# Optimization experiments

Hardware: AMD Instinct MI355X
Metric: run time of the kernel (lower is better)

The kernel has to match this reference:

```python
import jax, jax.numpy as jnp
import numpy as np

DIM = 1024
NQ = 16
NKV = 4
HD = DIM // NQ  # 64
HID = 2048
E = 8
B, S = 1, 1024
EPS = 1e-6


def rmsnorm(x, w):
    ms = jnp.mean(x * x, axis=-1, keepdims=True)
    return w * (x * jax.lax.rsqrt(ms + EPS))


def rope_tables(seq_len, head_dim):
    inv_freq = 1.0 / (10000.0 ** (jnp.arange(0, head_dim, 2, dtype=jnp.float32) / head_dim))
    t = jnp.arange(seq_len, dtype=jnp.float32)
    freqs = jnp.einsum('i,j->ij', t, inv_freq)  # [S, HD/2]
    return jnp.cos(freqs), jnp.sin(freqs)


def apply_rope(x, cos, sin):
    # x: [B, S, H, HD]; cos/sin: [S, HD/2]
    c = cos[None, :, None, :]
    s = sin[None, :, None, :]
    half = x.shape[-1] // 2
    x1, x2 = x[..., :half], x[..., half:]
    return jnp.concatenate([x1 * c - x2 * s, x1 * s + x2 * c], axis=-1)


def setup_inputs() -> dict:
    key = jax.random.key(0)
    ks = jax.random.split(key, 20)
    sc = lambda fan_in: 1.0 / np.sqrt(fan_in)
    d = {}
    d['x'] = jax.random.normal(ks[0], (B, S, DIM), dtype=jnp.float32)
    d['ln1_w'] = jnp.ones((DIM,), jnp.float32)
    d['ln2_w'] = jnp.ones((DIM,), jnp.float32)
    d['Wq'] = jax.random.normal(ks[1], (DIM, DIM), jnp.float32) * sc(DIM)
    d['bq'] = jnp.zeros((DIM,), jnp.float32)
    d['Wk'] = jax.random.normal(ks[2], (DIM, HD * NKV), jnp.float32) * sc(DIM)
    d['bk'] = jnp.zeros((HD * NKV,), jnp.float32)
    d['Wv'] = jax.random.normal(ks[3], (DIM, HD * NKV), jnp.float32) * sc(DIM)
    d['bv'] = jnp.zeros((HD * NKV,), jnp.float32)
    d['qn_w'] = jnp.ones((HD,), jnp.float32)
    d['kn_w'] = jnp.ones((HD,), jnp.float32)
    d['Wg'] = jax.random.normal(ks[4], (HD, HD), jnp.float32) * sc(HD)
    d['bg'] = jnp.zeros((HD,), jnp.float32)
    d['Wo'] = jax.random.normal(ks[5], (DIM, DIM), jnp.float32) * sc(DIM)
    d['bo'] = jnp.zeros((DIM,), jnp.float32)
    d['Wr'] = jax.random.normal(ks[6], (DIM, E), jnp.float32) * sc(DIM)
    d['br'] = jnp.zeros((E,), jnp.float32)
    d['W1'] = jax.random.normal(ks[7], (E, DIM, 2 * HID), jnp.float32) * sc(DIM)
    d['b1'] = jnp.zeros((E, 2 * HID), jnp.float32)
    d['W2'] = jax.random.normal(ks[8], (E, HID, DIM), jnp.float32) * sc(HID)
    d['b2'] = jnp.zeros((E, DIM), jnp.float32)
    return d


def _forward(x, ln1_w, ln2_w, Wq, bq, Wk, bk, Wv, bv, qn_w, kn_w, Wg, bg, Wo, bo,
             Wr, br, W1, b1, W2, b2):
    batch, seq, _ = x.shape
    cos, sin = rope_tables(seq, HD)

    # --- attention ---
    h = rmsnorm(x, ln1_w)
    q = (h @ Wq + bq).reshape(batch, seq, NQ, HD)
    k = (h @ Wk + bk).reshape(batch, seq, NKV, HD)
    v = (h @ Wv + bv).reshape(batch, seq, NKV, HD)
    q = rmsnorm(apply_rope(q, cos, sin), qn_w)
    k = rmsnorm(apply_rope(k, cos, sin), kn_w)
    rep = NQ // NKV
    k = jnp.repeat(k, rep, axis=2)  # [B,S,NQ,HD]
    v = jnp.repeat(v, rep, axis=2)
    scores = jnp.einsum('bthd,bshd->bhts', q, k) / np.sqrt(HD)
    causal = jnp.tril(jnp.ones((seq, seq), dtype=bool))
    scores = jnp.where(causal[None, None], scores, -jnp.inf)
    attn = jax.nn.softmax(scores, axis=-1)
    out = jnp.einsum('bhts,bshd->bthd', attn, v)
    gate = jax.nn.sigmoid(out @ Wg + bg)
    out = (out * gate).reshape(batch, seq, DIM)
    x = x + out @ Wo + bo

    # --- top-1 MoE (note: output is NOT scaled by router probs) ---
    h2 = rmsnorm(x, ln2_w)
    logits = h2 @ Wr + br  # [B,S,E]
    top1 = jnp.argmax(logits, axis=-1).reshape(-1)  # [T]
    xt = h2.reshape(-1, DIM)  # [T,DIM]
    # dense dispatch: run all experts, gather the chosen one
    u = jnp.einsum('td,edf->tef', xt, W1) + b1  # [T,E,2H]
    u1, u2 = u[..., :HID], u[..., HID:]
    act = u1 * jax.nn.sigmoid(u2)  # SwiGLU
    y_all = jnp.einsum('teh,ehd->ted', act, W2) + b2  # [T,E,DIM]
    y = jnp.take_along_axis(y_all, top1[:, None, None], axis=1)[:, 0, :]
    return x + y.reshape(batch, seq, DIM)


def reference(x, ln1_w, ln2_w, Wq, bq, Wk, bk, Wv, bv, qn_w, kn_w, Wg, bg, Wo, bo,
              Wr, br, W1, b1, W2, b2):
    return _forward(x, ln1_w, ln2_w, Wq, bq, Wk, bk, Wv, bv, qn_w, kn_w,
                    Wg, bg, Wo, bo, Wr, br, W1, b1, W2, b2)
```

## Files before the change

### kernel.cpp

```cpp
#include <hip/hip_runtime.h>
#include <hip/hip_bf16.h>
#include <cstddef>

#define DIM 1024
#define NQ 16
#define NKV 4
#define HD 64
#define HID 2048
#define NE 8
#define SEQ 1024
#define EPSF 1e-6f
#define MAX_TILES 24
#define GST 72

typedef __hip_bfloat16 bf16;
typedef __attribute__((ext_vector_type(8))) short short8;
typedef __attribute__((ext_vector_type(4))) float floatx4;

typedef union { short8 s; unsigned int u[4]; } s8u;

__device__ __forceinline__ unsigned int f2b(float f) {
    union { bf16 b; unsigned short s; } u;
    u.b = __float2bfloat16(f);
    return (unsigned int)u.s;
}
__device__ __forceinline__ unsigned int pk2(float a, float b) {
    return f2b(a) | (f2b(b) << 16);
}

__global__ __launch_bounds__(256) void rmsnorm_kernel(const float* __restrict__ src,
                                                      const float* __restrict__ w,
                                                      float* __restrict__ dst)
{
    int row = blockIdx.x, tid = threadIdx.x;
    __shared__ float red[256];
    float vals[4];
    float sq = 0.f;
    size_t base = (size_t)row * DIM;
    #pragma unroll
    for (int i = 0; i < 4; i++) {
        int idx = tid + i * 256;
        float v = src[base + idx];
        vals[i] = v; sq += v * v;
    }
    red[tid] = sq; __syncthreads();
    for (int s = 128; s > 0; s >>= 1) {
        if (tid < s) red[tid] += red[tid + s];
        __syncthreads();
    }
    float rs = 1.0f / sqrtf(red[0] * (1.0f / DIM) + EPSF);
    #pragma unroll
    for (int i = 0; i < 4; i++) {
        int idx = tid + i * 256;
        dst[base + idx] = w[idx] * vals[i] * rs;
    }
}

__global__ __launch_bounds__(256) void gemm_kernel(
    const float* __restrict__ A, const float* __restrict__ B, const float* __restrict__ bias,
    float* __restrict__ C, const float* __restrict__ resf,
    const int* __restrict__ perm, const int* __restrict__ tile_expert,
    int N, int K, int mode)
{
    __shared__ short As[64 * GST];
    __shared__ short Bs[64 * GST];
    int tid = threadIdx.x;
    int mbase = blockIdx.y * 64, nbase = blockIdx.x * 64;

    size_t Beoff = 0, biasoff = 0;
    if (tile_expert) {
        int e = tile_expert[blockIdx.y];
        if (e < 0) return;
        Beoff = (size_t)e * K * N;
        biasoff = (size_t)e * N;
    }

    int ar = tid >> 4, ak = (tid & 15) << 2;
    int bn = tid & 63, bkk = (tid >> 6) << 4;
    const float* BpBase = B + Beoff + (size_t)bkk * N + nbase + bn;

    int wv = tid >> 6, ln = tid & 63;
    int fm = (wv << 4) + (ln & 15);
    int fn = ln & 15;
    int fk = (ln >> 4) << 3;

    floatx4 acc[4];
    #pragma unroll
    for (int nt = 0; nt < 4; nt++)
        #pragma unroll
        for (int r = 0; r < 4; r++) acc[nt][r] = 0.f;

    float4 apre[4];
    float bpre[16];
    #pragma unroll
    for (int p = 0; p < 4; p++)
        apre[p] = *(const float4*)(A + (size_t)(mbase + (p << 4) + ar) * K + ak);
    #pragma unroll
    for (int i = 0; i < 16; i++)
        bpre[i] = BpBase[(size_t)i * N];

    for (int kt = 0; kt < K; kt += 64) {
        #pragma unroll
        for (int p = 0; p < 4; p++) {
            int m = (p << 4) + ar;
            uint2 wpk; wpk.x = pk2(apre[p].x, apre[p].y); wpk.y = pk2(apre[p].z, apre[p].w);
            *(uint2*)&As[m * GST + ak] = wpk;
        }
        {
            unsigned int u[8];
            #pragma unroll
            for (int i = 0; i < 8; i++) u[i] = pk2(bpre[2 * i], bpre[2 * i + 1]);
            *(uint4*)&Bs[bn * GST + bkk]     = make_uint4(u[0], u[1], u[2], u[3]);
            *(uint4*)&Bs[bn * GST + bkk + 8] = make_uint4(u[4], u[5], u[6], u[7]);
        }
        __syncthreads();

        int kn = kt + 64;
        if (kn < K) {
            #pragma unroll
            for (int p = 0; p < 4; p++)
                apre[p] = *(const float4*)(A + (size_t)(mbase + (p << 4) + ar) * K + kn + ak);
            const float* bp = BpBase + (size_t)kn * N;
            #pragma unroll
            for (int i = 0; i < 16; i++) bpre[i] = bp[(size_t)i * N];
        }

        #pragma unroll
        for (int ks = 0; ks < 2; ks++) {
            short8 af = *(const short8*)&As[fm * GST + (ks << 5) + fk];
            #pragma unroll
            for (int nt = 0; nt < 4; nt++) {
                short8 bf = *(const short8*)&Bs[((nt << 4) + fn) * GST + (ks << 5) + fk];
                acc[nt] = __builtin_amdgcn_mfma_f32_16x16x32_bf16(af, bf, acc[nt], 0, 0, 0);
            }
        }
        __syncthreads();
    }

    int rowb = mbase + (wv << 4) + ((ln >> 4) << 2);
    if (mode == 2) {
        int tk[4];
        #pragma unroll
        for (int r = 0; r < 4; r++) tk[r] = perm[rowb + r];
        #pragma unroll
        for (int nt = 0; nt < 4; nt++) {
            int col = nbase + (nt << 4) + fn;
            float bsv = bias[biasoff + col];
            #pragma unroll
            for (int r = 0; r < 4; r++)
                if (tk[r] >= 0)
                    C[(size_t)tk[r] * N + col] = resf[(size_t)tk[r] * N + col] + acc[nt][r] + bsv;
        }
    } else {
        #pragma unroll
        for (int nt = 0; nt < 4; nt++) {
            int col = nbase + (nt << 4) + fn;
            float bsv = bias[col];
            #pragma unroll
            for (int r = 0; r < 4; r++) {
                float vv = acc[nt][r] + bsv;
                if (mode == 1) vv += resf[(size_t)(rowb + r) * N + col];
                C[(size_t)(rowb + r) * N + col] = vv;
            }
        }
    }
}

__global__ __launch_bounds__(256) void qkv_kernel(
    const float* __restrict__ A,
    const float* __restrict__ Wq, const float* __restrict__ bq,
    const float* __restrict__ Wk, const float* __restrict__ bk,
    const float* __restrict__ Wv, const float* __restrict__ bv,
    float* __restrict__ qo, float* __restrict__ ko, float* __restrict__ vo)
{
    __shared__ short As[64 * GST];
    __shared__ short Bs[64 * GST];
    int tid = threadIdx.x;
    int bx = blockIdx.x;
    int mbase = blockIdx.y * 64;

    const float* B; const float* bias; float* C; int N, nbase;
    if (bx < 16)      { B = Wq; bias = bq; C = qo; N = DIM;      nbase = bx * 64; }
    else if (bx < 20) { B = Wk; bias = bk; C = ko; N = NKV * HD; nbase = (bx - 16) * 64; }
    else              { B = Wv; bias = bv; C = vo; N = NKV * HD; nbase = (bx - 20) * 64; }

    int ar = tid >> 4, ak = (tid & 15) << 2;
    int bn = tid & 63, bkk = (tid >> 6) << 4;
    const float* BpBase = B + (size_t)bkk * N + nbase + bn;

    int wv = tid >> 6, ln = tid & 63;
    int fm = (wv << 4) + (ln & 15);
    int fn = ln & 15;
    int fk = (ln >> 4) << 3;

    floatx4 acc[4];
    #pragma unroll
    for (int nt = 0; nt < 4; nt++)
        #pragma unroll
        for (int r = 0; r < 4; r++) acc[nt][r] = 0.f;

    float4 apre[4];
    float bpre[16];
    #pragma unroll
    for (int p = 0; p < 4; p++)
        apre[p] = *(const float4*)(A + (size_t)(mbase + (p << 4) + ar) * DIM + ak);
    #pragma unroll
    for (int i = 0; i < 16; i++)
        bpre[i] = BpBase[(size_t)i * N];

    for (int kt = 0; kt < DIM; kt += 64) {
        #pragma unroll
        for (int p = 0; p < 4; p++) {
            int m = (p << 4) + ar;
            uint2 wpk; wpk.x = pk2(apre[p].x, apre[p].y); wpk.y = pk2(apre[p].z, apre[p].w);
            *(uint2*)&As[m * GST + ak] = wpk;
        }
        {
            unsigned int u[8];
            #pragma unroll
            for (int i = 0; i < 8; i++) u[i] = pk2(bpre[2 * i], bpre[2 * i + 1]);
            *(uint4*)&Bs[bn * GST + bkk]     = make_uint4(u[0], u[1], u[2], u[3]);
            *(uint4*)&Bs[bn * GST + bkk + 8] = make_uint4(u[4], u[5], u[6], u[7]);
        }
        __syncthreads();

        int kn = kt + 64;
        if (kn < DIM) {
            #pragma unroll
            for (int p = 0; p < 4; p++)
                apre[p] = *(const float4*)(A + (size_t)(mbase + (p << 4) + ar) * DIM + kn + ak);
            const float* bp = BpBase + (size_t)kn * N;
            #pragma unroll
            for (int i = 0; i < 16; i++) bpre[i] = bp[(size_t)i * N];
        }

        #pragma unroll
        for (int ks = 0; ks < 2; ks++) {
            short8 af = *(const short8*)&As[fm * GST + (ks << 5) + fk];
            #pragma unroll
            for (int nt = 0; nt < 4; nt++) {
                short8 bf = *(const short8*)&Bs[((nt << 4) + fn) * GST + (ks << 5) + fk];
                acc[nt] = __builtin_amdgcn_mfma_f32_16x16x32_bf16(af, bf, acc[nt], 0, 0, 0);
            }
        }
        __syncthreads();
    }

    int rowb = mbase + (wv << 4) + ((ln >> 4) << 2);
    #pragma unroll
    for (int nt = 0; nt < 4; nt++) {
        int col = nbase + (nt << 4) + fn;
        float bsv = bias[col];
        #pragma unroll
        for (int r = 0; r < 4; r++)
            C[(size_t)(rowb + r) * N + col] = acc[nt][r] + bsv;
    }
}

__global__ __launch_bounds__(256) void moe1_kernel(
    const float* __restrict__ A,
    const float* __restrict__ W1,
    const float* __restrict__ b1,
    float* __restrict__ act,
    const int* __restrict__ perm,
    const int* __restrict__ tile_expert)
{
    __shared__ short As[64 * GST];
    __shared__ short B1s[64 * GST];
    __shared__ short B2s[64 * GST];
    int tid = threadIdx.x;
    int mbase = blockIdx.y * 64, nbase = blockIdx.x * 64;
    int e = tile_expert[blockIdx.y];
    if (e < 0) return;
    const float* Wp = W1 + (size_t)e * DIM * (2 * HID);
    const float* bp1 = b1 + (size_t)e * (2 * HID);

    int ar = tid >> 4, ak = (tid & 15) << 2;
    int tok[4];
    #pragma unroll
    for (int p = 0; p < 4; p++) tok[p] = perm[mbase + (p << 4) + ar];

    int bn = tid & 63, bkk = (tid >> 6) << 4;
    const float* BpBase = Wp + (size_t)bkk * (2 * HID) + nbase + bn;

    int wv = tid >> 6, ln = tid & 63;
    int fm = (wv << 4) + (ln & 15);
    int fn = ln & 15;
    int fk = (ln >> 4) << 3;

    floatx4 acc1[4], acc2[4];
    #pragma unroll
    for (int nt = 0; nt < 4; nt++)
        #pragma unroll
        for (int r = 0; r < 4; r++) { acc1[nt][r] = 0.f; acc2[nt][r] = 0.f; }

    float4 apre[4];
    float b1pre[16], b2pre[16];
    #pragma unroll
    for (int p = 0; p < 4; p++)
        apre[p] = (tok[p] >= 0)
            ? *(const float4*)(A + (size_t)tok[p] * DIM + ak)
            : make_float4(0.f, 0.f, 0.f, 0.f);
    #pragma unroll
    for (int i = 0; i < 16; i++) {
        b1pre[i] = BpBase[(size_t)i * (2 * HID)];
        b2pre[i] = BpBase[(size_t)i * (2 * HID) + HID];
    }

    for (int kt = 0; kt < DIM; kt += 64) {
        #pragma unroll
        for (int p = 0; p < 4; p++) {
            int m = (p << 4) + ar;
            uint2 wpk; wpk.x = pk2(apre[p].x, apre[p].y); wpk.y = pk2(apre[p].z, apre[p].w);
            *(uint2*)&As[m * GST + ak] = wpk;
        }
        {
            unsigned int u1[8], u2[8];
            #pragma unroll
            for (int i = 0; i < 8; i++) {
                u1[i] = pk2(b1pre[2 * i], b1pre[2 * i + 1]);
                u2[i] = pk2(b2pre[2 * i], b2pre[2 * i + 1]);
            }
            *(uint4*)&B1s[bn * GST + bkk]     = make_uint4(u1[0], u1[1], u1[2], u1[3]);
            *(uint4*)&B1s[bn * GST + bkk + 8] = make_uint4(u1[4], u1[5], u1[6], u1[7]);
            *(uint4*)&B2s[bn * GST + bkk]     = make_uint4(u2[0], u2[1], u2[2], u2[3]);
            *(uint4*)&B2s[bn * GST + bkk + 8] = make_uint4(u2[4], u2[5], u2[6], u2[7]);
        }
        __syncthreads();

        int kn = kt + 64;
        if (kn < DIM) {
            #pragma unroll
            for (int p = 0; p < 4; p++)
                apre[p] = (tok[p] >= 0)
                    ? *(const float4*)(A + (size_t)tok[p] * DIM + kn + ak)
                    : make_float4(0.f, 0.f, 0.f, 0.f);
            const float* bp = BpBase + (size_t)kn * (2 * HID);
            #pragma unroll
            for (int i = 0; i < 16; i++) {
                b1pre[i] = bp[(size_t)i * (2 * HID)];
                b2pre[i] = bp[(size_t)i * (2 * HID) + HID];
            }
        }

        #pragma unroll
        for (int ks = 0; ks < 2; ks++) {
            short8 af = *(const short8*)&As[fm * GST + (ks << 5) + fk];
            #pragma unroll
            for (int nt = 0; nt < 4; nt++) {
                int bo = ((nt << 4) + fn) * GST + (ks << 5) + fk;
                short8 bf1 = *(const short8*)&B1s[bo];
                short8 bf2 = *(const short8*)&B2s[bo];
                acc1[nt] = __builtin_amdgcn_mfma_f32_16x16x32_bf16(af, bf1, acc1[nt], 0, 0, 0);
                acc2[nt] = __builtin_amdgcn_mfma_f32_16x16x32_bf16(af, bf2, acc2[nt], 0, 0, 0);
            }
        }
        __syncthreads();
    }

    int rowb = mbase + (wv << 4) + ((ln >> 4) << 2);
    #pragma unroll
    for (int nt = 0; nt < 4; nt++) {
        int col = nbase + (nt << 4) + fn;
        float bs1 = bp1[col];
        float bs2 = bp1[HID + col];
        #pragma unroll
        for (int r = 0; r < 4; r++) {
            float u1 = acc1[nt][r] + bs1;
            float u2 = acc2[nt][r] + bs2;
            act[(size_t)(rowb + r) * HID + col] = u1 * (1.0f / (1.0f + expf(-u2)));
        }
    }
}

__global__ __launch_bounds__(64) void rope_rms_kernel(float* __restrict__ x,
                                                      const float* __restrict__ w, int nh)
{
    int t = blockIdx.x, h = blockIdx.y, d = threadIdx.x;
    int base = (t * nh + h) * HD;
    int i = d & 31;
    float x1 = x[base + i];
    float x2 = x[base + 32 + i];
    float inv = 1.0f / powf(10000.0f, (float)(2 * i) * (1.0f / HD));
    float fr = (float)t * inv;
    float c = cosf(fr), s = sinf(fr);
    float r = (d < 32) ? (x1 * c - x2 * s) : (x1 * s + x2 * c);
    float sq = r * r;
    #pragma unroll
    for (int m = 32; m >= 1; m >>= 1) sq += __shfl_xor(sq, m);
    float rs = 1.0f / sqrtf(sq * (1.0f / HD) + EPSF);
    __syncthreads();
    x[base + d] = r * rs * w[d];
}

__global__ __launch_bounds__(256) void fattn_kernel(const float* __restrict__ q,
                                                    const float* __restrict__ k,
                                                    const float* __restrict__ v,
                                                    float* __restrict__ o)
{
    __shared__ short lds[2][2][64 * GST];

    int h = blockIdx.x, qt = blockIdx.y;
    int kvh = h >> 2;
    int tid = threadIdx.x;
    int w = tid >> 6, ln = tid & 63;
    int c = ln & 15, g = ln >> 4;
    int qbase = qt * 64;
    const size_t krow = (size_t)NKV * HD;

    short8 qf[2];
    {
        const float* qp = q + ((size_t)(qbase + 16 * w + c) * NQ + h) * HD + 8 * g;
        #pragma unroll
        for (int ks = 0; ks < 2; ks++) {
            float4 a = *(const float4*)(qp + 32 * ks);
            float4 b = *(const float4*)(qp + 32 * ks + 4);
            s8u t;
            t.u[0] = pk2(a.x * 0.125f, a.y * 0.125f);
            t.u[1] = pk2(a.z * 0.125f, a.w * 0.125f);
            t.u[2] = pk2(b.x * 0.125f, b.y * 0.125f);
            t.u[3] = pk2(b.z * 0.125f, b.w * 0.125f);
            qf[ks] = t.s;
        }
    }

    int kr[4], kd4[4];
    #pragma unroll
    for (int i = 0; i < 4; i++) { int f4 = tid + 256 * i; kr[i] = f4 >> 4; kd4[i] = f4 & 15; }
    int vd = tid & 63, vrb = (tid >> 6) << 4;

    float4 kreg[4];
    float vreg[16];
    {
        const float* kb = k + (size_t)kvh * HD;
        #pragma unroll
        for (int i = 0; i < 4; i++)
            kreg[i] = *(const float4*)(kb + (size_t)kr[i] * krow + kd4[i] * 4);
        const float* vb = v + (size_t)kvh * HD + vd;
        #pragma unroll
        for (int i = 0; i < 16; i++)
            vreg[i] = vb[(size_t)(vrb + i) * krow];
    }

    float m_i = -INFINITY, l_i = 0.f;
    floatx4 ot[4];
    #pragma unroll
    for (int mt = 0; mt < 4; mt++)
        #pragma unroll
        for (int r = 0; r < 4; r++) ot[mt][r] = 0.f;

    for (int kt = 0; kt <= qt; kt++) {
        short* KB = lds[kt & 1][0];
        short* VT = lds[kt & 1][1];

        #pragma unroll
        for (int i = 0; i < 4; i++) {
            uint2 wp; wp.x = pk2(kreg[i].x, kreg[i].y); wp.y = pk2(kreg[i].z, kreg[i].w);
            *(uint2*)&KB[kr[i] * GST + kd4[i] * 4] = wp;
        }
        {
            unsigned int u[8];
            #pragma unroll
            for (int i = 0; i < 8; i++) u[i] = pk2(vreg[2 * i], vreg[2 * i + 1]);
            *(uint4*)&VT[vd * GST + vrb]     = make_uint4(u[0], u[1], u[2], u[3]);
            *(uint4*)&VT[vd * GST + vrb + 8] = make_uint4(u[4], u[5], u[6], u[7]);
        }
        __syncthreads();

        if (kt < qt) {
            int kb2 = (kt + 1) * 64;
            const float* kb = k + ((size_t)kb2 * NKV + kvh) * HD;
            #pragma unroll
            for (int i = 0; i < 4; i++)
                kreg[i] = *(const float4*)(kb + (size_t)kr[i] * krow + kd4[i] * 4);
            const float* vp = v + ((size_t)kb2 * NKV + kvh) * HD + vd;
            #pragma unroll
            for (int i = 0; i < 16; i++)
                vreg[i] = vp[(size_t)(vrb + i) * krow];
        }

        float p[4][4];
        #pragma unroll
        for (int mt = 0; mt < 4; mt++) {
            floatx4 s = {0.f, 0.f, 0.f, 0.f};
            #pragma unroll
            for (int ks = 0; ks < 2; ks++) {
                short8 kf = *(const short8*)&KB[(16 * mt + c) * GST + 32 * ks + 8 * g];
                s = __builtin_amdgcn_mfma_f32_16x16x32_bf16(kf, qf[ks], s, 0, 0, 0);
            }
            #pragma unroll
            for (int r = 0; r < 4; r++) p[mt][r] = s[r];
        }

        if (kt == qt) {
            #pragma unroll
            for (int mt = 0; mt < 4; mt++)
                #pragma unroll
                for (int r = 0; r < 4; r++)
                    if (16 * mt + 4 * g + r > 16 * w + c) p[mt][r] = -1e30f;
        }

        float tm = p[0][0];
        #pragma unroll
        for (int mt = 0; mt < 4; mt++)
            #pragma unroll
            for (int r = 0; r < 4; r++) tm = fmaxf(tm, p[mt][r]);
        tm = fmaxf(tm, __shfl_xor(tm, 16));
        tm = fmaxf(tm, __shfl_xor(tm, 32));
        float mn = fmaxf(m_i, tm);
        float alpha = __expf(m_i - mn);
        float ts = 0.f;
        #pragma unroll
        for (int mt = 0; mt < 4; mt++)
            #pragma unroll
            for (int r = 0; r < 4; r++) {
                float e = __expf(p[mt][r] - mn);
                p[mt][r] = e; ts += e;
            }
        ts += __shfl_xor(ts, 16);
        ts += __shfl_xor(ts, 32);
        l_i = alpha * l_i + ts;
        m_i = mn;
        #pragma unroll
        for (int mt = 0; mt < 4; mt++)
            #pragma unroll
            for (int r = 0; r < 4; r++) ot[mt][r] *= alpha;

        unsigned int pd[4][2];
        #pragma unroll
        for (int mt = 0; mt < 4; mt++) {
            pd[mt][0] = pk2(p[mt][0], p[mt][1]);
            pd[mt][1] = pk2(p[mt][2], p[mt][3]);
        }

        int srcA = c + ((ln & 16) << 1);
        int srcB = srcA + 16;
        int gh = g >> 1;
        short8 pf[2];
        #pragma unroll
        for (int ks = 0; ks < 2; ks++) {
            s8u t;
            unsigned int a0 = (unsigned)__shfl((int)pd[2 * ks][0],     srcA);
            unsigned int a1 = (unsigned)__shfl((int)pd[2 * ks + 1][0], srcA);
            t.u[0] = gh ? a1 : a0;
            unsigned int b0 = (unsigned)__shfl((int)pd[2 * ks][1],     srcA);
            unsigned int b1 = (unsigned)__shfl((int)pd[2 * ks + 1][1], srcA);
            t.u[1] = gh ? b1 : b0;
            unsigned int c0 = (unsigned)__shfl((int)pd[2 * ks][0],     srcB);
            unsigned int c1 = (unsigned)__shfl((int)pd[2 * ks + 1][0], srcB);
            t.u[2] = gh ? c1 : c0;
            unsigned int d0 = (unsigned)__shfl((int)pd[2 * ks][1],     srcB);
            unsigned int d1 = (unsigned)__shfl((int)pd[2 * ks + 1][1], srcB);
            t.u[3] = gh ? d1 : d0;
            pf[ks] = t.s;
        }

        #pragma unroll
        for (int mt = 0; mt < 4; mt++) {
            #pragma unroll
            for (int ks = 0; ks < 2; ks++) {
                short8 vf = *(const short8*)&VT[(16 * mt + c) * GST + 32 * ks + 8 * g];
                ot[mt] = __builtin_amdgcn_mfma_f32_16x16x32_bf16(vf, pf[ks], ot[mt], 0, 0, 0);
            }
        }
    }

    __syncthreads();
    float* OT = (float*)lds;
    float rl = 1.0f / l_i;
    #pragma unroll
    for (int mt = 0; mt < 4; mt++)
        #pragma unroll
        for (int r = 0; r < 4; r++)
            OT[(16 * w + c) * 68 + 16 * mt + 4 * g + r] = ot[mt][r] * rl;
    __syncthreads();
    #pragma unroll
    for (int i = 0; i < 4; i++) {
        int idx = tid + 256 * i;
        int rq = idx >> 4, d4 = idx & 15;
        float4 val = *(const float4*)&OT[rq * 68 + d4 * 4];
        *(float4*)(o + ((size_t)(qbase + rq) * NQ + h) * HD + d4 * 4) = val;
    }
}

__global__ __launch_bounds__(64) void gate_kernel(float* __restrict__ o,
                                                  const float* __restrict__ Wg,
                                                  const float* __restrict__ bg)
{
    int t = blockIdx.x, h = blockIdx.y, d = threadIdx.x;
    __shared__ float ao[HD];
    int base = (t * NQ + h) * HD;
    ao[d] = o[base + d];
    __syncthreads();
    float acc = bg[d];
    #pragma unroll 8
    for (int e = 0; e < HD; e++) acc += ao[e] * Wg[e * HD + d];
    float g = 1.0f / (1.0f + expf(-acc));
    o[base + d] = ao[d] * g;
}

__global__ __launch_bounds__(64) void router_kernel(const float* __restrict__ h2,
                                                    const float* __restrict__ Wr,
                                                    const float* __restrict__ br,
                                                    int* __restrict__ top1)
{
    int t = blockIdx.x, lane = threadIdx.x;
    float acc[NE] = {0.f, 0.f, 0.f, 0.f, 0.f, 0.f, 0.f, 0.f};
    for (int d = lane; d < DIM; d += 64) {
        float hv = h2[(size_t)t * DIM + d];
        float4 w0 = *(const float4*)(Wr + (size_t)d * NE);
        float4 w1 = *(const float4*)(Wr + (size_t)d * NE + 4);
        acc[0] += hv * w0.x; acc[1] += hv * w0.y;
        acc[2] += hv * w0.z; acc[3] += hv * w0.w;
        acc[4] += hv * w1.x; acc[5] += hv * w1.y;
        acc[6] += hv * w1.z; acc[7] += hv * w1.w;
    }
    #pragma unroll
    for (int e = 0; e < NE; e++)
        for (int off = 32; off >= 1; off >>= 1) acc[e] += __shfl_down(acc[e], off);
    if (lane == 0) {
        float best = acc[0] + br[0]; int be = 0;
        #pragma unroll
        for (int e = 1; e < NE; e++) {
            float l = acc[e] + br[e];
            if (l > best) { best = l; be = e; }
        }
        top1[t] = be;
    }
}

__global__ __launch_bounds__(64) void bucket_kernel(const int* __restrict__ top1,
                                                    int* __restrict__ perm,
                                                    int* __restrict__ tile_expert)
{
    int lane = threadIdx.x;

    int e_of[16];
    {
        const int4* tp = (const int4*)(top1 + lane * 16);
        #pragma unroll
        for (int c = 0; c < 4; c++) {
            int4 v = tp[c];
            e_of[c * 4 + 0] = v.x & 7;
            e_of[c * 4 + 1] = v.y & 7;
            e_of[c * 4 + 2] = v.z & 7;
            e_of[c * 4 + 3] = v.w & 7;
        }
    }

    int cnt[NE];
    #pragma unroll
    for (int e = 0; e < NE; e++) {
        int c = 0;
        #pragma unroll
        for (int i = 0; i < 16; i++) c += (e_of[i] == e) ? 1 : 0;
        cnt[e] = c;
    }

    int pre[NE];
    #pragma unroll
    for (int e = 0; e < NE; e++) pre[e] = cnt[e];
    #pragma unroll
    for (int off = 1; off < 64; off <<= 1) {
        #pragma unroll
        for (int e = 0; e < NE; e++) {
            int t = __shfl_up(pre[e], off);
            if (lane >= off) pre[e] += t;
        }
    }
    int tot[NE];
    #pragma unroll
    for (int e = 0; e < NE; e++) {
        tot[e] = __shfl(pre[e], 63);
        pre[e] -= cnt[e];
    }

    int off_e[NE + 1];
    off_e[0] = 0;
    #pragma unroll
    for (int e = 0; e < NE; e++)
        off_e[e + 1] = off_e[e] + (((tot[e] + 63) >> 6) << 6);

    if (lane < MAX_TILES) {
        int tb = lane << 6;
        int te = -1;
        #pragma unroll
        for (int e = 0; e < NE; e++)
            if (tb >= off_e[e] && tb < off_e[e + 1]) te = e;
        tile_expert[lane] = te;
    }

    #pragma unroll
    for (int e = 0; e < NE; e++)
        for (int i = off_e[e] + tot[e] + lane; i < off_e[e + 1]; i += 64)
            perm[i] = -1;

    #pragma unroll
    for (int e = 0; e < NE; e++) {
        int pos = off_e[e] + pre[e];
        #pragma unroll
        for (int i = 0; i < 16; i++) {
            if (e_of[i] == e) { perm[pos] = lane * 16 + i; pos++; }
        }
    }
}

extern "C" void kernel_launch(void* const* d_in, const int* in_sizes, int n_in,
                              void* d_out, int out_size, void* d_ws, size_t ws_size,
                              hipStream_t stream)
{
    const float* x    = (const float*)d_in[0];
    const float* ln1w = (const float*)d_in[1];
    const float* ln2w = (const float*)d_in[2];
    const float* Wq   = (const float*)d_in[3];
    const float* bq   = (const float*)d_in[4];
    const float* Wk   = (const float*)d_in[5];
    const float* bk   = (const float*)d_in[6];
    const float* Wv   = (const float*)d_in[7];
    const float* bv   = (const float*)d_in[8];
    const float* qnw  = (const float*)d_in[9];
    const float* knw  = (const float*)d_in[10];
    const float* Wg   = (const float*)d_in[11];
    const float* bg   = (const float*)d_in[12];
    const float* Wo   = (const float*)d_in[13];
    const float* bo   = (const float*)d_in[14];
    const float* Wr   = (const float*)d_in[15];
    const float* br   = (const float*)d_in[16];
    const float* W1   = (const float*)d_in[17];
    const float* b1   = (const float*)d_in[18];
    const float* W2   = (const float*)d_in[19];
    const float* b2   = (const float*)d_in[20];
    float* out = (float*)d_out;
    (void)in_sizes; (void)n_in; (void)out_size; (void)ws_size;

    char* ws = (char*)d_ws;
    float* h    = (float*)(ws);
    float* q    = (float*)(ws + ((size_t)4  << 20));
    float* kbuf = (float*)(ws + ((size_t)8  << 20));
    float* vbuf = (float*)(ws + ((size_t)9  << 20));
    float* ao   = (float*)(ws + ((size_t)10 << 20));
    float* x2   = (float*)(ws);
    float* h2   = (float*)(ws + ((size_t)4  << 20));
    float* act  = (float*)(ws + ((size_t)8  << 20));
    int* top1   = (int*)  (ws + ((size_t)20 << 20));
    int* perm   = top1 + 2048;
    int* texp   = perm + MAX_TILES * 64;

    rmsnorm_kernel<<<SEQ, 256, 0, stream>>>(x, ln1w, h);
    qkv_kernel<<<dim3(24, SEQ / 64), 256, 0, stream>>>(
        h, Wq, bq, Wk, bk, Wv, bv, q, kbuf, vbuf);
    rope_rms_kernel<<<dim3(SEQ, NQ),  64, 0, stream>>>(q,    qnw, NQ);
    rope_rms_kernel<<<dim3(SEQ, NKV), 64, 0, stream>>>(kbuf, knw, NKV);
    fattn_kernel<<<dim3(NQ, SEQ / 64), 256, 0, stream>>>(q, kbuf, vbuf, ao);
    gate_kernel<<<dim3(SEQ, NQ), 64, 0, stream>>>(ao, Wg, bg);
    gemm_kernel<<<dim3(DIM / 64, SEQ / 64), 256, 0, stream>>>(
        ao, Wo, bo, x2, x, nullptr, nullptr, DIM, DIM, 1);
    rmsnorm_kernel<<<SEQ, 256, 0, stream>>>(x2, ln2w, h2);
    router_kernel<<<SEQ, 64, 0, stream>>>(h2, Wr, br, top1);
    bucket_kernel<<<1, 64, 0, stream>>>(top1, perm, texp);
    moe1_kernel<<<dim3(HID / 64, MAX_TILES), 256, 0, stream>>>(
        h2, W1, b1, act, perm, texp);
    gemm_kernel<<<dim3(DIM / 64, MAX_TILES), 256, 0, stream>>>(
        act, W2, b2, out, x2, perm, texp, DIM, HID, 2);
}
```

Before: 436.9 us.

## Halve GEMM N-tiles to 32, fuse gate into attention, merge q/k rope launches

Every GEMM-style kernel (qkv, Wo, moe1, moe2) now uses 32-wide N tiles instead of 64, so the grids have twice as many blocks and fill more compute units at this small token count. The sigmoid gate projection moves into the attention epilogue through an LDS-staged Wg, which removes a separate kernel and one round trip of the attention output through memory. The two rope/RMS launches for q and k become one launch. The act/top1 workspace offsets also move, likely to avoid overlap. In exchange, each block reuses A less, and attention blocks do extra serial FMA work in the epilogue.

```diff
diff --git a/kernel.cpp b/kernel.cpp
--- a/kernel.cpp
+++ b/kernel.cpp
@@ -56,16 +56,19 @@
     }
 }
 
-__global__ __launch_bounds__(256) void gemm_kernel(
+template<int NB>
+__global__ __launch_bounds__(256) void gemm_t(
     const float* __restrict__ A, const float* __restrict__ B, const float* __restrict__ bias,
     float* __restrict__ C, const float* __restrict__ resf,
     const int* __restrict__ perm, const int* __restrict__ tile_expert,
     int N, int K, int mode)
 {
+    constexpr int KR = NB / 4;
+    constexpr int NT = NB / 16;
     __shared__ short As[64 * GST];
-    __shared__ short Bs[64 * GST];
+    __shared__ short Bs[NB * GST];
     int tid = threadIdx.x;
-    int mbase = blockIdx.y * 64, nbase = blockIdx.x * 64;
+    int mbase = blockIdx.y * 64, nbase = blockIdx.x * NB;
 
     size_t Beoff = 0, biasoff = 0;
     if (tile_expert) {
@@ -76,7 +79,7 @@
     }
 
     int ar = tid >> 4, ak = (tid & 15) << 2;
-    int bn = tid & 63, bkk = (tid >> 6) << 4;
+    int bn = tid & (NB - 1), bkk = (tid / NB) * KR;
     const float* BpBase = B + Beoff + (size_t)bkk * N + nbase + bn;
 
     int wv = tid >> 6, ln = tid & 63;
@@ -84,19 +87,19 @@
     int fn = ln & 15;
     int fk = (ln >> 4) << 3;
 
-    floatx4 acc[4];
-    #pragma unroll
-    for (int nt = 0; nt < 4; nt++)
+    floatx4 acc[NT];
+    #pragma unroll
+    for (int nt = 0; nt < NT; nt++)
         #pragma unroll
         for (int r = 0; r < 4; r++) acc[nt][r] = 0.f;
 
     float4 apre[4];
-    float bpre[16];
+    float bpre[KR];
     #pragma unroll
     for (int p = 0; p < 4; p++)
         apre[p] = *(const float4*)(A + (size_t)(mbase + (p << 4) + ar) * K + ak);
     #pragma unroll
-    for (int i = 0; i < 16; i++)
+    for (int i = 0; i < KR; i++)
         bpre[i] = BpBase[(size_t)i * N];
 
     for (int kt = 0; kt < K; kt += 64) {
@@ -106,12 +109,13 @@
             uint2 wpk; wpk.x = pk2(apre[p].x, apre[p].y); wpk.y = pk2(apre[p].z, apre[p].w);
             *(uint2*)&As[m * GST + ak] = wpk;
         }
-        {
-            unsigned int u[8];
-            #pragma unroll
-            for (int i = 0; i < 8; i++) u[i] = pk2(bpre[2 * i], bpre[2 * i + 1]);
-            *(uint4*)&Bs[bn * GST + bkk]     = make_uint4(u[0], u[1], u[2], u[3]);
-            *(uint4*)&Bs[bn * GST + bkk + 8] = make_uint4(u[4], u[5], u[6], u[7]);
+        #pragma unroll
+        for (int i2 = 0; i2 < KR; i2 += 8) {
+            unsigned int u[4];
+            #pragma unroll
+            for (int i = 0; i < 4; i++)
+                u[i] = pk2(bpre[i2 + 2 * i], bpre[i2 + 2 * i + 1]);
+            *(uint4*)&Bs[bn * GST + bkk + i2] = make_uint4(u[0], u[1], u[2], u[3]);
         }
         __syncthreads();
 
@@ -122,14 +126,14 @@
                 apre[p] = *(const float4*)(A + (size_t)(mbase + (p << 4) + ar) * K + kn + ak);
             const float* bp = BpBase + (size_t)kn * N;
             #pragma unroll
-            for (int i = 0; i < 16; i++) bpre[i] = bp[(size_t)i * N];
+            for (int i = 0; i < KR; i++) bpre[i] = bp[(size_t)i * N];
         }
 
         #pragma unroll
         for (int ks = 0; ks < 2; ks++) {
             short8 af = *(const short8*)&As[fm * GST + (ks << 5) + fk];
             #pragma unroll
-            for (int nt = 0; nt < 4; nt++) {
+            for (int nt = 0; nt < NT; nt++) {
                 short8 bf = *(const short8*)&Bs[((nt << 4) + fn) * GST + (ks << 5) + fk];
                 acc[nt] = __builtin_amdgcn_mfma_f32_16x16x32_bf16(af, bf, acc[nt], 0, 0, 0);
             }
@@ -143,7 +147,7 @@
         #pragma unroll
         for (int r = 0; r < 4; r++) tk[r] = perm[rowb + r];
         #pragma unroll
-        for (int nt = 0; nt < 4; nt++) {
+        for (int nt = 0; nt < NT; nt++) {
             int col = nbase + (nt << 4) + fn;
             float bsv = bias[biasoff + col];
             #pragma unroll
@@ -153,7 +157,7 @@
         }
     } else {
         #pragma unroll
-        for (int nt = 0; nt < 4; nt++) {
+        for (int nt = 0; nt < NT; nt++) {
             int col = nbase + (nt << 4) + fn;
             float bsv = bias[col];
             #pragma unroll
@@ -173,19 +177,20 @@
     const float* __restrict__ Wv, const float* __restrict__ bv,
     float* __restrict__ qo, float* __restrict__ ko, float* __restrict__ vo)
 {
+    constexpr int NB = 32, KR = 8, NT = 2;
     __shared__ short As[64 * GST];
-    __shared__ short Bs[64 * GST];
+    __shared__ short Bs[NB * GST];
     int tid = threadIdx.x;
     int bx = blockIdx.x;
     int mbase = blockIdx.y * 64;
 
     const float* B; const float* bias; float* C; int N, nbase;
-    if (bx < 16)      { B = Wq; bias = bq; C = qo; N = DIM;      nbase = bx * 64; }
-    else if (bx < 20) { B = Wk; bias = bk; C = ko; N = NKV * HD; nbase = (bx - 16) * 64; }
-    else              { B = Wv; bias = bv; C = vo; N = NKV * HD; nbase = (bx - 20) * 64; }
+    if (bx < 32)      { B = Wq; bias = bq; C = qo; N = DIM;      nbase = bx * 32; }
+    else if (bx < 40) { B = Wk; bias = bk; C = ko; N = NKV * HD; nbase = (bx - 32) * 32; }
+    else              { B = Wv; bias = bv; C = vo; N = NKV * HD; nbase = (bx - 40) * 32; }
 
     int ar = tid >> 4, ak = (tid & 15) << 2;
-    int bn = tid & 63, bkk = (tid >> 6) << 4;
+    int bn = tid & (NB - 1), bkk = (tid / NB) * KR;
     const float* BpBase = B + (size_t)bkk * N + nbase + bn;
 
     int wv = tid >> 6, ln = tid & 63;
@@ -193,19 +198,19 @@
     int fn = ln & 15;
     int fk = (ln >> 4) << 3;
 
-    floatx4 acc[4];
-    #pragma unroll
-    for (int nt = 0; nt < 4; nt++)
+    floatx4 acc[NT];
+    #pragma unroll
+    for (int nt = 0; nt < NT; nt++)
         #pragma unroll
         for (int r = 0; r < 4; r++) acc[nt][r] = 0.f;
 
     float4 apre[4];
-    float bpre[16];
+    float bpre[KR];
     #pragma unroll
     for (int p = 0; p < 4; p++)
         apre[p] = *(const float4*)(A + (size_t)(mbase + (p << 4) + ar) * DIM + ak);
     #pragma unroll
-    for (int i = 0; i < 16; i++)
+    for (int i = 0; i < KR; i++)
         bpre[i] = BpBase[(size_t)i * N];
 
     for (int kt = 0; kt < DIM; kt += 64) {
@@ -216,11 +221,11 @@
             *(uint2*)&As[m * GST + ak] = wpk;
         }
         {
-            unsigned int u[8];
-            #pragma unroll
-            for (int i = 0; i < 8; i++) u[i] = pk2(bpre[2 * i], bpre[2 * i + 1]);
-            *(uint4*)&Bs[bn * GST + bkk]     = make_uint4(u[0], u[1], u[2], u[3]);
-            *(uint4*)&Bs[bn * GST + bkk + 8] = make_uint4(u[4], u[5], u[6], u[7]);
+            unsigned int u[4];
+            #pragma unroll
+            for (int i = 0; i < 4; i++)
+                u[i] = pk2(bpre[2 * i], bpre[2 * i + 1]);
+            *(uint4*)&Bs[bn * GST + bkk] = make_uint4(u[0], u[1], u[2], u[3]);
         }
         __syncthreads();
 
@@ -231,14 +236,14 @@
                 apre[p] = *(const float4*)(A + (size_t)(mbase + (p << 4) + ar) * DIM + kn + ak);
             const float* bp = BpBase + (size_t)kn * N;
             #pragma unroll
-            for (int i = 0; i < 16; i++) bpre[i] = bp[(size_t)i * N];
+            for (int i = 0; i < KR; i++) bpre[i] = bp[(size_t)i * N];
         }
 
         #pragma unroll
         for (int ks = 0; ks < 2; ks++) {
             short8 af = *(const short8*)&As[fm * GST + (ks << 5) + fk];
             #pragma unroll
-            for (int nt = 0; nt < 4; nt++) {
+            for (int nt = 0; nt < NT; nt++) {
                 short8 bf = *(const short8*)&Bs[((nt << 4) + fn) * GST + (ks << 5) + fk];
                 acc[nt] = __builtin_amdgcn_mfma_f32_16x16x32_bf16(af, bf, acc[nt], 0, 0, 0);
             }
@@ -248,7 +253,7 @@
 
     int rowb = mbase + (wv << 4) + ((ln >> 4) << 2);
     #pragma unroll
-    for (int nt = 0; nt < 4; nt++) {
+    for (int nt = 0; nt < NT; nt++) {
         int col = nbase + (nt << 4) + fn;
         float bsv = bias[col];
         #pragma unroll
@@ -265,11 +270,12 @@
     const int* __restrict__ perm,
     const int* __restrict__ tile_expert)
 {
+    constexpr int NB = 32, KR = 8, NT = 2;
     __shared__ short As[64 * GST];
-    __shared__ short B1s[64 * GST];
-    __shared__ short B2s[64 * GST];
+    __shared__ short B1s[NB * GST];
+    __shared__ short B2s[NB * GST];
     int tid = threadIdx.x;
-    int mbase = blockIdx.y * 64, nbase = blockIdx.x * 64;
+    int mbase = blockIdx.y * 64, nbase = blockIdx.x * NB;
     int e = tile_expert[blockIdx.y];
     if (e < 0) return;
     const float* Wp = W1 + (size_t)e * DIM * (2 * HID);
@@ -280,7 +286,7 @@
     #pragma unroll
     for (int p = 0; p < 4; p++) tok[p] = perm[mbase + (p << 4) + ar];
 
-    int bn = tid & 63, bkk = (tid >> 6) << 4;
+    int bn = tid & (NB - 1), bkk = (tid / NB) * KR;
     const float* BpBase = Wp + (size_t)bkk * (2 * HID) + nbase + bn;
 
     int wv = tid >> 6, ln = tid & 63;
@@ -288,21 +294,21 @@
     int fn = ln & 15;
     int fk = (ln >> 4) << 3;
 
-    floatx4 acc1[4], acc2[4];
-    #pragma unroll
-    for (int nt = 0; nt < 4; nt++)
+    floatx4 acc1[NT], acc2[NT];
+    #pragma unroll
+    for (int nt = 0; nt < NT; nt++)
         #pragma unroll
         for (int r = 0; r < 4; r++) { acc1[nt][r] = 0.f; acc2[nt][r] = 0.f; }
 
     float4 apre[4];
-    float b1pre[16], b2pre[16];
+    float b1pre[KR], b2pre[KR];
     #pragma unroll
     for (int p = 0; p < 4; p++)
         apre[p] = (tok[p] >= 0)
             ? *(const float4*)(A + (size_t)tok[p] * DIM + ak)
             : make_float4(0.f, 0.f, 0.f, 0.f);
     #pragma unroll
-    for (int i = 0; i < 16; i++) {
+    for (int i = 0; i < KR; i++) {
         b1pre[i] = BpBase[(size_t)i * (2 * HID)];
         b2pre[i] = BpBase[(size_t)i * (2 * HID) + HID];
     }
@@ -315,16 +321,14 @@
             *(uint2*)&As[m * GST + ak] = wpk;
         }
         {
-            unsigned int u1[8], u2[8];
-            #pragma unroll
-            for (int i = 0; i < 8; i++) {
+            unsigned int u1[4], u2[4];
+            #pragma unroll
+            for (int i = 0; i < 4; i++) {
                 u1[i] = pk2(b1pre[2 * i], b1pre[2 * i + 1]);
                 u2[i] = pk2(b2pre[2 * i], b2pre[2 * i + 1]);
             }
-            *(uint4*)&B1s[bn * GST + bkk]     = make_uint4(u1[0], u1[1], u1[2], u1[3]);
-            *(uint4*)&B1s[bn * GST + bkk + 8] = make_uint4(u1[4], u1[5], u1[6], u1[7]);
-            *(uint4*)&B2s[bn * GST + bkk]     = make_uint4(u2[0], u2[1], u2[2], u2[3]);
-            *(uint4*)&B2s[bn * GST + bkk + 8] = make_uint4(u2[4], u2[5], u2[6], u2[7]);
+            *(uint4*)&B1s[bn * GST + bkk] = make_uint4(u1[0], u1[1], u1[2], u1[3]);
+            *(uint4*)&B2s[bn * GST + bkk] = make_uint4(u2[0], u2[1], u2[2], u2[3]);
         }
         __syncthreads();
 
@@ -337,7 +341,7 @@
                     : make_float4(0.f, 0.f, 0.f, 0.f);
             const float* bp = BpBase + (size_t)kn * (2 * HID);
             #pragma unroll
-            for (int i = 0; i < 16; i++) {
+            for (int i = 0; i < KR; i++) {
                 b1pre[i] = bp[(size_t)i * (2 * HID)];
                 b2pre[i] = bp[(size_t)i * (2 * HID) + HID];
             }
@@ -347,7 +351,7 @@
         for (int ks = 0; ks < 2; ks++) {
             short8 af = *(const short8*)&As[fm * GST + (ks << 5) + fk];
             #pragma unroll
-            for (int nt = 0; nt < 4; nt++) {
+            for (int nt = 0; nt < NT; nt++) {
                 int bo = ((nt << 4) + fn) * GST + (ks << 5) + fk;
                 short8 bf1 = *(const short8*)&B1s[bo];
                 short8 bf2 = *(const short8*)&B2s[bo];
@@ -360,7 +364,7 @@
 
     int rowb = mbase + (wv << 4) + ((ln >> 4) << 2);
     #pragma unroll
-    for (int nt = 0; nt < 4; nt++) {
+    for (int nt = 0; nt < NT; nt++) {
         int col = nbase + (nt << 4) + fn;
         float bs1 = bp1[col];
         float bs2 = bp1[HID + col];
@@ -373,10 +377,15 @@
     }
 }
 
-__global__ __launch_bounds__(64) void rope_rms_kernel(float* __restrict__ x,
-                                                      const float* __restrict__ w, int nh)
-{
-    int t = blockIdx.x, h = blockIdx.y, d = threadIdx.x;
+__global__ __launch_bounds__(64) void rope_rms_kernel(float* __restrict__ qb,
+                                                      float* __restrict__ kb,
+                                                      const float* __restrict__ qnw,
+                                                      const float* __restrict__ knw)
+{
+    int t = blockIdx.x, hy = blockIdx.y, d = threadIdx.x;
+    float* x; const float* w; int nh, h;
+    if (hy < NQ) { x = qb; w = qnw; nh = NQ;  h = hy; }
+    else         { x = kb; w = knw; nh = NKV; h = hy - NQ; }
     int base = (t * nh + h) * HD;
     int i = d & 31;
     float x1 = x[base + i];
@@ -396,6 +405,8 @@
 __global__ __launch_bounds__(256) void fattn_kernel(const float* __restrict__ q,
                                                     const float* __restrict__ k,
                                                     const float* __restrict__ v,
+                                                    const float* __restrict__ Wg,
+                                                    const float* __restrict__ bg,
                                                     float* __restrict__ o)
 {
     __shared__ short lds[2][2][64 * GST];
@@ -566,37 +577,54 @@
     }
 
     __syncthreads();
-    float* OT = (float*)lds;
+    float* L   = (float*)lds;
+    float* WgS = L + 64 * 68;
+
+    int we = tid >> 2, wd = (tid & 3) << 4;
+    float4 wg4[4];
+    #pragma unroll
+    for (int i = 0; i < 4; i++)
+        wg4[i] = *(const float4*)(Wg + (size_t)we * HD + wd + 4 * i);
+
     float rl = 1.0f / l_i;
     #pragma unroll
     for (int mt = 0; mt < 4; mt++)
         #pragma unroll
         for (int r = 0; r < 4; r++)
-            OT[(16 * w + c) * 68 + 16 * mt + 4 * g + r] = ot[mt][r] * rl;
+            L[(16 * w + c) * 68 + 16 * mt + 4 * g + r] = ot[mt][r] * rl;
+    #pragma unroll
+    for (int i = 0; i < 4; i++)
+        *(float4*)&WgS[we * 68 + wd + 4 * i] = wg4[i];
     __syncthreads();
+
+    int r = tid >> 2, d0 = (tid & 3) << 4;
+    float4 a0 = *(const float4*)(bg + d0);
+    float4 a1 = *(const float4*)(bg + d0 + 4);
+    float4 a2 = *(const float4*)(bg + d0 + 8);
+    float4 a3 = *(const float4*)(bg + d0 + 12);
+    for (int e = 0; e < HD; e++) {
+        float ov = L[r * 68 + e];
+        float4 w0 = *(const float4*)&WgS[e * 68 + d0];
+        float4 w1 = *(const float4*)&WgS[e * 68 + d0 + 4];
+        float4 w2 = *(const float4*)&WgS[e * 68 + d0 + 8];
+        float4 w3 = *(const float4*)&WgS[e * 68 + d0 + 12];
+        a0.x += ov * w0.x; a0.y += ov * w0.y; a0.z += ov * w0.z; a0.w += ov * w0.w;
+        a1.x += ov * w1.x; a1.y += ov * w1.y; a1.z += ov * w1.z; a1.w += ov * w1.w;
+        a2.x += ov * w2.x; a2.y += ov * w2.y; a2.z += ov * w2.z; a2.w += ov * w2.w;
+        a3.x += ov * w3.x; a3.y += ov * w3.y; a3.z += ov * w3.z; a3.w += ov * w3.w;
+    }
+    float* op = o + ((size_t)(qbase + r) * NQ + h) * HD + d0;
+    float4 av[4] = {a0, a1, a2, a3};
     #pragma unroll
     for (int i = 0; i < 4; i++) {
-        int idx = tid + 256 * i;
-        int rq = idx >> 4, d4 = idx & 15;
-        float4 val = *(const float4*)&OT[rq * 68 + d4 * 4];
-        *(float4*)(o + ((size_t)(qbase + rq) * NQ + h) * HD + d4 * 4) = val;
-    }
-}
-
-__global__ __launch_bounds__(64) void gate_kernel(float* __restrict__ o,
-                                                  const float* __restrict__ Wg,
-                                                  const float* __restrict__ bg)
-{
-    int t = blockIdx.x, h = blockIdx.y, d = threadIdx.x;
-    __shared__ float ao[HD];
-    int base = (t * NQ + h) * HD;
-    ao[d] = o[base + d];
-    __syncthreads();
-    float acc = bg[d];
-    #pragma unroll 8
-    for (int e = 0; e < HD; e++) acc += ao[e] * Wg[e * HD + d];
-    float g = 1.0f / (1.0f + expf(-acc));
-    o[base + d] = ao[d] * g;
+        float4 ov4 = *(const float4*)&L[r * 68 + d0 + 4 * i];
+        float4 res;
+        res.x = ov4.x / (1.0f + expf(-av[i].x));
+        res.y = ov4.y / (1.0f + expf(-av[i].y));
+        res.z = ov4.z / (1.0f + expf(-av[i].z));
+        res.w = ov4.w / (1.0f + expf(-av[i].w));
+        *(float4*)(op + 4 * i) = res;
+    }
 }
 
 __global__ __launch_bounds__(64) void router_kernel(const float* __restrict__ h2,
@@ -741,25 +769,23 @@
     float* ao   = (float*)(ws + ((size_t)10 << 20));
     float* x2   = (float*)(ws);
     float* h2   = (float*)(ws + ((size_t)4  << 20));
-    float* act  = (float*)(ws + ((size_t)8  << 20));
-    int* top1   = (int*)  (ws + ((size_t)20 << 20));
+    float* act  = (float*)(ws + ((size_t)24 << 20));
+    int* top1   = (int*)  (ws + ((size_t)44 << 20));
     int* perm   = top1 + 2048;
     int* texp   = perm + MAX_TILES * 64;
 
     rmsnorm_kernel<<<SEQ, 256, 0, stream>>>(x, ln1w, h);
-    qkv_kernel<<<dim3(24, SEQ / 64), 256, 0, stream>>>(
+    qkv_kernel<<<dim3(48, SEQ / 64), 256, 0, stream>>>(
         h, Wq, bq, Wk, bk, Wv, bv, q, kbuf, vbuf);
-    rope_rms_kernel<<<dim3(SEQ, NQ),  64, 0, stream>>>(q,    qnw, NQ);
-    rope_rms_kernel<<<dim3(SEQ, NKV), 64, 0, stream>>>(kbuf, knw, NKV);
-    fattn_kernel<<<dim3(NQ, SEQ / 64), 256, 0, stream>>>(q, kbuf, vbuf, ao);
-    gate_kernel<<<dim3(SEQ, NQ), 64, 0, stream>>>(ao, Wg, bg);
-    gemm_kernel<<<dim3(DIM / 64, SEQ / 64), 256, 0, stream>>>(
+    rope_rms_kernel<<<dim3(SEQ, NQ + NKV), 64, 0, stream>>>(q, kbuf, qnw, knw);
+    fattn_kernel<<<dim3(NQ, SEQ / 64), 256, 0, stream>>>(q, kbuf, vbuf, Wg, bg, ao);
+    gemm_t<32><<<dim3(DIM / 32, SEQ / 64), 256, 0, stream>>>(
         ao, Wo, bo, x2, x, nullptr, nullptr, DIM, DIM, 1);
     rmsnorm_kernel<<<SEQ, 256, 0, stream>>>(x2, ln2w, h2);
     router_kernel<<<SEQ, 64, 0, stream>>>(h2, Wr, br, top1);
     bucket_kernel<<<1, 64, 0, stream>>>(top1, perm, texp);
-    moe1_kernel<<<dim3(HID / 64, MAX_TILES), 256, 0, stream>>>(
+    moe1_kernel<<<dim3(HID / 32, MAX_TILES), 256, 0, stream>>>(
         h2, W1, b1, act, perm, texp);
-    gemm_kernel<<<dim3(DIM / 64, MAX_TILES), 256, 0, stream>>>(
+    gemm_t<32><<<dim3(DIM / 32, MAX_TILES), 256, 0, stream>>>(
         act, W2, b2, out, x2, perm, texp, DIM, HID, 2);
 }
```

Result: no change. 438.4 us (+0.3%).
